# Kernel tuning notes

Measured on AMD Instinct MI355X. Metric: run time of the kernel, lower is better.

## Reference

```python
import jax, jax.numpy as jnp
import numpy as np

D_MODEL = 256; N_LEVELS = 4; N_HEADS = 8; N_POINTS = 4
H_SP = 32; W_SP = 32
B = 2; LEN_Q = 1024; LEN_IN = N_LEVELS * H_SP * W_SP
D_HEAD = D_MODEL // N_HEADS
K9 = 9 * N_POINTS  # 3x3 neighborhood around each of the top-k matches


def setup_inputs() -> dict:
    key = jax.random.key(0)
    k1, k2, k3, k4 = jax.random.split(key, 4)
    bound = (6.0 / (D_MODEL + D_MODEL)) ** 0.5  # xavier_uniform for output_proj
    return {
        "query": jax.random.normal(k1, (B, LEN_Q, D_MODEL), jnp.float32),
        "reference_points": jax.random.uniform(k2, (B, LEN_Q, N_LEVELS, 2), dtype=jnp.float32),
        "input_flatten": jax.random.normal(k3, (B, LEN_IN, D_MODEL), jnp.float32),
        # all levels share the same h==w==32 spatial shape (required by the module)
        "input_spatial_shapes": np.full((N_LEVELS, 2), H_SP, dtype=np.int64),
        "input_level_start_index": (np.arange(N_LEVELS) * H_SP * W_SP).astype(np.int64),
        "out_proj_w": jax.random.uniform(k4, (D_MODEL, D_MODEL), jnp.float32, -bound, bound),
        "out_proj_b": jnp.zeros((D_MODEL,), jnp.float32),
    }


def _sample_offset(query, input_flatten, h, w, t):
    # per-head correlation -> softmax -> top-k index -> 3x3 neighborhood -> (x,y) offsets
    n, lq, _ = query.shape
    q = query.reshape(n, lq, N_HEADS, D_HEAD)
    v = input_flatten.reshape(n, -1, N_HEADS, D_HEAD)
    corr = jnp.einsum('nqhd,nkhd->nhqk', q, v) / D_HEAD          # [n,H,lq,Lin]
    corr = corr.reshape(n, N_HEADS, lq, t, h * w)
    prob = jax.nn.softmax(10.0 * corr, axis=-1)
    _, idx = jax.lax.top_k(prob, N_POINTS)                        # [n,H,lq,t,P] int32
    deltas = jnp.array([-1 - h, -h, 1 - h, -1, 0, 1, -1 + h, h, 1 + h], jnp.int32)
    # torch cat order is delta-major: all P points for delta1, then delta2, ...
    res = (idx[..., None, :] + deltas[:, None]).reshape(n, N_HEADS, lq, t, K9)
    res = jnp.clip(res, 0, (h - 1) * (w - 1))                     # faithful (h-1)*(w-1) clamp
    resf = res.astype(jnp.float32)
    off_w = jnp.floor(resf / h)
    off_h = resf - off_w * h
    offsets = jnp.stack([off_w, off_h], axis=-1)                  # [n,H,lq,t,K9,2]
    return jnp.transpose(offsets, (0, 2, 1, 3, 4, 5))             # [n,lq,H,L,K9,2]


def _ms_deform_attn(value, loc, h, w):
    # value [n,Lin,H,dh]; loc in [0,1], [n,lq,H,L,K9,2]; grid_sample-style bilinear, zero pad
    n, lq = loc.shape[0], loc.shape[1]
    v = value.reshape(n, N_LEVELS, h * w, N_HEADS, D_HEAD)
    v = jnp.transpose(v, (0, 3, 1, 2, 4))                         # [n,H,L,hw,dh]
    x = loc[..., 0] * w - 0.5
    y = loc[..., 1] * h - 0.5
    x0 = jnp.floor(x); y0 = jnp.floor(y)
    lw = x - x0; lh = y - y0
    attn_w = 1.0 / (N_LEVELS * K9)  # softmax of all-ones buffer is uniform
    acc = jnp.zeros((n, lq, N_HEADS, D_HEAD), jnp.float32)
    corners = ((y0, x0, (1 - lh) * (1 - lw)), (y0, x0 + 1, (1 - lh) * lw),
               (y0 + 1, x0, lh * (1 - lw)), (y0 + 1, x0 + 1, lh * lw))
    for yi, xi, wgt in corners:
        valid = (yi >= 0) & (yi < h) & (xi >= 0) & (xi < w)
        ii = (jnp.clip(yi, 0, h - 1) * w + jnp.clip(xi, 0, w - 1)).astype(jnp.int32)
        ww = jnp.where(valid, wgt, 0.0) * attn_w                  # [n,lq,H,L,K9]
        ii_t = jnp.transpose(ii, (0, 2, 3, 1, 4)).reshape(n, N_HEADS, N_LEVELS, lq * K9)
        g = jnp.take_along_axis(v, ii_t[..., None], axis=3)       # [n,H,L,lq*K9,dh]
        g = g.reshape(n, N_HEADS, N_LEVELS, lq, K9, D_HEAD)
        ww_t = jnp.transpose(ww, (0, 2, 3, 1, 4))                 # [n,H,L,lq,K9]
        acc = acc + jnp.einsum('nhlqk,nhlqkd->nqhd', ww_t, g)
    return acc.reshape(n, lq, D_MODEL)


def reference(query, reference_points, input_flatten, input_spatial_shapes,
              input_level_start_index, out_proj_w, out_proj_b):
    ss = np.asarray(input_spatial_shapes)
    h = int(ss[0, 0]); w = h
    lin = input_flatten.shape[1]
    t = lin // (h * w)  # == N_LEVELS
    value = input_flatten.reshape(input_flatten.shape[0], lin, N_HEADS, D_HEAD)
    offsets = _sample_offset(query, input_flatten, h, w, t)
    assert reference_points.shape[-1] == 2
    normalizer = jnp.asarray(np.stack([ss[:, 1], ss[:, 0]], -1), jnp.float32)  # [L,2]=(w,h)
    loc = offsets / normalizer[None, None, None, :, None, :]
    out = _ms_deform_attn(value, loc, h, w)
    out = out @ out_proj_w.T + out_proj_b
    return out, loc
```

## Files before the change

kernel.cpp:

```cpp
#include <hip/hip_runtime.h>
#include <math.h>

#define BB 2
#define LQ 1024
#define DM 256
#define NH 8
#define DH 32
#define NL 4
#define HWsp 1024
#define LIN 4096
#define K9 36
#define NGRP (BB * NH * NL * LQ)

typedef short bf16x8 __attribute__((ext_vector_type(8)));
typedef float f32x4 __attribute__((ext_vector_type(4)));

__device__ __forceinline__ ushort bf16rn(float x) {
  unsigned u = __float_as_uint(x);
  unsigned r = (u + 0x7FFFu + ((u >> 16) & 1u)) >> 16;
  return (ushort)r;
}
__device__ __forceinline__ float bf16tof(ushort h) {
  return __uint_as_float(((unsigned)h) << 16);
}

#define INSERT4(val, index)                                              \
  {                                                                      \
    const float v_ = (val);                                              \
    const int ix_ = (index);                                             \
    if (v_ > v3) {                                                       \
      if (v_ > v1) {                                                     \
        if (v_ > v0) {                                                   \
          v3 = v2; i3 = i2; v2 = v1; i2 = i1; v1 = v0; i1 = i0;          \
          v0 = v_; i0 = ix_;                                             \
        } else {                                                         \
          v3 = v2; i3 = i2; v2 = v1; i2 = i1; v1 = v_; i1 = ix_;         \
        }                                                                \
      } else {                                                           \
        if (v_ > v2) {                                                   \
          v3 = v2; i3 = i2; v2 = v_; i2 = ix_;                           \
        } else {                                                         \
          v3 = v_; i3 = ix_;                                             \
        }                                                                \
      }                                                                  \
    }                                                                    \
  }

#define LEXGT(v_, ix_, vv, ii) (((v_) > (vv)) || ((v_) == (vv) && (ix_) < (ii)))

#define INSERT4LEX(val, index)                                               \
  {                                                                          \
    const float v_ = (val);                                                  \
    const int ix_ = (index);                                                 \
    if (LEXGT(v_, ix_, rv3, ri3)) {                                          \
      if (LEXGT(v_, ix_, rv1, ri1)) {                                        \
        if (LEXGT(v_, ix_, rv0, ri0)) {                                      \
          rv3 = rv2; ri3 = ri2; rv2 = rv1; ri2 = ri1; rv1 = rv0; ri1 = ri0;  \
          rv0 = v_; ri0 = ix_;                                               \
        } else {                                                             \
          rv3 = rv2; ri3 = ri2; rv2 = rv1; ri2 = ri1; rv1 = v_; ri1 = ix_;   \
        }                                                                    \
      } else {                                                               \
        if (LEXGT(v_, ix_, rv2, ri2)) {                                      \
          rv3 = rv2; ri3 = ri2; rv2 = v_; ri2 = ix_;                         \
        } else {                                                             \
          rv3 = v_; ri3 = ix_;                                               \
        }                                                                    \
      }                                                                      \
    }                                                                        \
  }

#define LMAX(av, ai, bv, bi)                                        \
  {                                                                 \
    const bool g_ = ((av) > (bv)) || ((av) == (bv) && (ai) < (bi)); \
    if (!g_) { (av) = (bv); (ai) = (bi); }                          \
  }
#define CEX(av, ai, bv, bi)                                         \
  {                                                                 \
    const bool g_ = ((av) > (bv)) || ((av) == (bv) && (ai) < (bi)); \
    const float tv_ = g_ ? (av) : (bv);                             \
    const int ti_ = g_ ? (ai) : (bi);                               \
    (bv) = g_ ? (bv) : (av); (bi) = g_ ? (bi) : (ai);               \
    (av) = tv_; (ai) = ti_;                                         \
  }

#define PSTRIDE ((size_t)BB * NL * NH * 1024 * 32)

__global__ __launch_bounds__(256) void vsplit_kernel(
    const float* __restrict__ value, ushort* __restrict__ vs) {
  const int T = blockIdx.x * 256 + threadIdx.x;
  const int flat = T << 3;
  const int n = flat >> 20;
  const int rem = flat & 0xFFFFF;
  const int lin = rem >> 8;
  const int d0 = rem & 255;
  const int l = lin >> 10, row = lin & 1023;
  const int h = d0 >> 5, dd = d0 & 31;

  const float* src = value + (size_t)flat;
  float xf[8];
  *(float4*)&xf[0] = *(const float4*)src;
  *(float4*)&xf[4] = *(const float4*)(src + 4);

  ushort uh[8], ul[8], ul2[8];
  #pragma unroll
  for (int j = 0; j < 8; ++j) {
    const float x = xf[j];
    const ushort h1 = bf16rn(x);
    const float r1 = x - bf16tof(h1);
    const ushort h2 = bf16rn(r1);
    const float r2 = r1 - bf16tof(h2);
    uh[j] = h1; ul[j] = h2; ul2[j] = bf16rn(r2);
  }
  const size_t ob = ((((size_t)((n * NL + l) * NH + h)) << 10) + row) * 32 + dd;
  *(bf16x8*)(vs + 0 * PSTRIDE + ob) =
      (bf16x8){(short)uh[0], (short)uh[1], (short)uh[2], (short)uh[3],
               (short)uh[4], (short)uh[5], (short)uh[6], (short)uh[7]};
  *(bf16x8*)(vs + 1 * PSTRIDE + ob) =
      (bf16x8){(short)ul[0], (short)ul[1], (short)ul[2], (short)ul[3],
               (short)ul[4], (short)ul[5], (short)ul[6], (short)ul[7]};
  *(bf16x8*)(vs + 2 * PSTRIDE + ob) =
      (bf16x8){(short)ul2[0], (short)ul2[1], (short)ul2[2], (short)ul2[3],
               (short)ul2[4], (short)ul2[5], (short)ul2[6], (short)ul2[7]};
}

template <int SPLIT, int PRESPLIT>
__global__ __launch_bounds__(256) void corr_topk_kernel(
    const float* __restrict__ query, const float* __restrict__ value,
    const ushort* __restrict__ vs, int* __restrict__ idx_out,
    float4* __restrict__ pval, int4* __restrict__ pidx) {
  __shared__ ushort hiL[64][32];
  __shared__ ushort loL[64][32];
  __shared__ ushort lo2L[64][32];

  const int tid = threadIdx.x;
  const int nh = blockIdx.z;
  const int n = nh >> 3, h = nh & 7;
  const int l = blockIdx.y;
  const int qc = (SPLIT == 2) ? ((int)blockIdx.x >> 1) : (int)blockIdx.x;
  const int half = (SPLIT == 2) ? ((int)blockIdx.x & 1) : 0;
  const int c0 = (SPLIT == 2) ? (half << 3) : 0;
  const int c1 = (SPLIT == 2) ? (c0 + 8) : 16;
  const int w = tid >> 6, L = tid & 63;
  const int qtile = (qc << 2) + w;
  const int r16 = L & 15, g = L >> 4;

  float qf[8];
  bf16x8 qhi, qlo, qlo2;
  {
    const float* qp =
        query + (size_t)(n * LQ + (qtile << 4) + r16) * DM + h * DH + (g << 3);
    *(float4*)&qf[0] = *(const float4*)qp;
    *(float4*)&qf[4] = *(const float4*)(qp + 4);
    ushort uh[8], ul[8], ul2[8];
    #pragma unroll
    for (int j = 0; j < 8; ++j) {
      const float x = qf[j];
      const ushort h1 = bf16rn(x);
      const float r1 = x - bf16tof(h1);
      const ushort h2 = bf16rn(r1);
      const float r2 = r1 - bf16tof(h2);
      uh[j] = h1; ul[j] = h2; ul2[j] = bf16rn(r2);
    }
    qhi = (bf16x8){(short)uh[0], (short)uh[1], (short)uh[2], (short)uh[3],
                   (short)uh[4], (short)uh[5], (short)uh[6], (short)uh[7]};
    qlo = (bf16x8){(short)ul[0], (short)ul[1], (short)ul[2], (short)ul[3],
                   (short)ul[4], (short)ul[5], (short)ul[6], (short)ul[7]};
    qlo2 = (bf16x8){(short)ul2[0], (short)ul2[1], (short)ul2[2], (short)ul2[3],
                    (short)ul2[4], (short)ul2[5], (short)ul2[6], (short)ul2[7]};
  }

  float v0 = -INFINITY, v1 = -INFINITY, v2 = -INFINITY, v3 = -INFINITY;
  int i0 = 0, i1 = 0, i2 = 0, i3 = 0;

  const int srow = tid >> 2, s = tid & 3;
  const int wslot = (s ^ ((srow >> 1) & 3)) << 3;
  const int rslot = (g ^ ((r16 >> 1) & 3)) << 3;
  const ushort* psbase =
      PRESPLIT ? vs + ((((size_t)((n * NL + l) * NH + h)) << 10)) * 32 : nullptr;
  const float* vbase = value + (size_t)(n * LIN + l * HWsp) * DM + h * DH;

  for (int c = c0; c < c1; ++c) {
    if (PRESPLIT) {
      const size_t off = ((size_t)((c << 6) + srow)) * 32 + (s << 3);
      *(bf16x8*)&hiL[srow][wslot] = *(const bf16x8*)(psbase + off);
      *(bf16x8*)&loL[srow][wslot] = *(const bf16x8*)(psbase + PSTRIDE + off);
      *(bf16x8*)&lo2L[srow][wslot] = *(const bf16x8*)(psbase + 2 * PSTRIDE + off);
    } else {
      const float* vp = vbase + (size_t)((c << 6) + srow) * DM + (s << 3);
      float xf[8];
      *(float4*)&xf[0] = *(const float4*)vp;
      *(float4*)&xf[4] = *(const float4*)(vp + 4);
      ushort uh[8], ul[8], ul2[8];
      #pragma unroll
      for (int j = 0; j < 8; ++j) {
        const float x = xf[j];
        const ushort h1 = bf16rn(x);
        const float r1 = x - bf16tof(h1);
        const ushort h2 = bf16rn(r1);
        const float r2 = r1 - bf16tof(h2);
        uh[j] = h1; ul[j] = h2; ul2[j] = bf16rn(r2);
      }
      *(bf16x8*)&hiL[srow][wslot] =
          (bf16x8){(short)uh[0], (short)uh[1], (short)uh[2], (short)uh[3],
                   (short)uh[4], (short)uh[5], (short)uh[6], (short)uh[7]};
      *(bf16x8*)&loL[srow][wslot] =
          (bf16x8){(short)ul[0], (short)ul[1], (short)ul[2], (short)ul[3],
                   (short)ul[4], (short)ul[5], (short)ul[6], (short)ul[7]};
      *(bf16x8*)&lo2L[srow][wslot] =
          (bf16x8){(short)ul2[0], (short)ul2[1], (short)ul2[2], (short)ul2[3],
                   (short)ul2[4], (short)ul2[5], (short)ul2[6], (short)ul2[7]};
    }
    __syncthreads();

    #pragma unroll
    for (int t = 0; t < 4; ++t) {
      const int row = (t << 4) + r16;
      const bf16x8 ahi = *(const bf16x8*)&hiL[row][rslot];
      const bf16x8 alo = *(const bf16x8*)&loL[row][rslot];
      const bf16x8 alo2 = *(const bf16x8*)&lo2L[row][rslot];
      f32x4 acc = {0.f, 0.f, 0.f, 0.f};
      acc = __builtin_amdgcn_mfma_f32_16x16x32_bf16(alo2, qhi, acc, 0, 0, 0);
      acc = __builtin_amdgcn_mfma_f32_16x16x32_bf16(ahi, qlo2, acc, 0, 0, 0);
      acc = __builtin_amdgcn_mfma_f32_16x16x32_bf16(alo, qlo, acc, 0, 0, 0);
      acc = __builtin_amdgcn_mfma_f32_16x16x32_bf16(alo, qhi, acc, 0, 0, 0);
      acc = __builtin_amdgcn_mfma_f32_16x16x32_bf16(ahi, qlo, acc, 0, 0, 0);
      acc = __builtin_amdgcn_mfma_f32_16x16x32_bf16(ahi, qhi, acc, 0, 0, 0);
      const float qm = fmaxf(fmaxf(acc[0], acc[1]), fmaxf(acc[2], acc[3]));
      const int qd = (c << 4) + (t << 2) + g;
      INSERT4(qm, qd);
    }
    __syncthreads();
  }

  #pragma unroll
  for (int m = 16; m < 64; m <<= 1) {
    const float b0 = __shfl_xor(v0, m);
    const float b1 = __shfl_xor(v1, m);
    const float b2 = __shfl_xor(v2, m);
    const float b3 = __shfl_xor(v3, m);
    const int j0 = __shfl_xor(i0, m);
    const int j1 = __shfl_xor(i1, m);
    const int j2 = __shfl_xor(i2, m);
    const int j3 = __shfl_xor(i3, m);
    LMAX(v0, i0, b3, j3);
    LMAX(v1, i1, b2, j2);
    LMAX(v2, i2, b1, j1);
    LMAX(v3, i3, b0, j0);
    CEX(v0, i0, v2, i2);
    CEX(v1, i1, v3, i3);
    CEX(v0, i0, v1, i1);
    CEX(v2, i2, v3, i3);
  }

  float rv0 = -INFINITY, rv1 = -INFINITY, rv2 = -INFINITY, rv3 = -INFINITY;
  int ri0 = 0, ri1 = 0, ri2 = 0, ri3 = 0;
  #define RECOVER_QUAD(QID)                                              \
    {                                                                    \
      _Pragma("unroll")                                                  \
      for (int j = 0; j < 4; ++j) {                                      \
        const int k = ((QID) << 2) + j;                                  \
        const float* vf = vbase + (size_t)k * DM + (g << 3);             \
        const float4 a0 = *(const float4*)vf;                            \
        const float4 a1 = *(const float4*)(vf + 4);                      \
        float p = qf[0] * a0.x;                                          \
        p = fmaf(qf[1], a0.y, p);                                        \
        p = fmaf(qf[2], a0.z, p);                                        \
        p = fmaf(qf[3], a0.w, p);                                        \
        p = fmaf(qf[4], a1.x, p);                                        \
        p = fmaf(qf[5], a1.y, p);                                        \
        p = fmaf(qf[6], a1.z, p);                                        \
        p = fmaf(qf[7], a1.w, p);                                        \
        p += __shfl_xor(p, 16);                                          \
        p += __shfl_xor(p, 32);                                          \
        INSERT4LEX(p, k);                                                \
      }                                                                  \
    }
  RECOVER_QUAD(i0)
  RECOVER_QUAD(i1)
  RECOVER_QUAD(i2)
  RECOVER_QUAD(i3)
  #undef RECOVER_QUAD

  if (L < 16) {
    const int q = (qtile << 4) + L;
    const size_t gi = (((size_t)nh * NL + l) << 10) + q;
    if (SPLIT == 2) {
      pval[gi * 2 + half] = make_float4(rv0, rv1, rv2, rv3);
      pidx[gi * 2 + half] = make_int4(ri0, ri1, ri2, ri3);
    } else {
      ((int4*)idx_out)[gi] = make_int4(ri0, ri1, ri2, ri3);
    }
  }
}

__global__ __launch_bounds__(256) void merge_topk_kernel(
    const float4* __restrict__ pval, const int4* __restrict__ pidx,
    int* __restrict__ idx_out) {
  const int t = blockIdx.x * 256 + threadIdx.x;
  const float4 av = pval[t * 2 + 0];
  const int4 ai = pidx[t * 2 + 0];
  const float4 bv = pval[t * 2 + 1];
  const int4 bi = pidx[t * 2 + 1];
  float w0 = av.x, w1 = av.y, w2 = av.z, w3 = av.w;
  int m0 = ai.x, m1 = ai.y, m2 = ai.z, m3 = ai.w;
  LMAX(w0, m0, bv.w, bi.w);
  LMAX(w1, m1, bv.z, bi.z);
  LMAX(w2, m2, bv.y, bi.y);
  LMAX(w3, m3, bv.x, bi.x);
  CEX(w0, m0, w2, m2);
  CEX(w1, m1, w3, m3);
  CEX(w0, m0, w1, m1);
  CEX(w2, m2, w3, m3);
  ((int4*)idx_out)[t] = make_int4(m0, m1, m2, m3);
}

__global__ __launch_bounds__(256) void loc_kernel(const int* __restrict__ idx_buf,
                                                  float* __restrict__ loc) {
  const int t = blockIdx.x * 256 + threadIdx.x;
  const int k = t % 36;
  int rest = t / 36;
  const int l = rest & 3; rest >>= 2;
  const int h = rest & 7; rest >>= 3;
  const int q = rest & 1023;
  const int n = rest >> 10;
  const int p = k & 3, dd = k >> 2;
  const int idx = idx_buf[(((((n << 3) + h) * NL + l) << 10) + q) * 4 + p];
  const int delta = ((dd / 3) - 1) * 32 + (dd % 3) - 1;
  int res = idx + delta;
  res = min(max(res, 0), 961);
  const int W = res >> 5, H = res & 31;
  ((float2*)loc)[t] = make_float2((float)W * 0.03125f, (float)H * 0.03125f);
}

__global__ __launch_bounds__(256) void gather_kernel(
    const float* __restrict__ value, const int* __restrict__ idx_buf,
    float* __restrict__ acc_out) {
  __shared__ float4 red[NL][8];
  const int bh = blockIdx.x;
  const int h = bh & 7;
  const int nq = bh >> 3;
  const int n = nq >> 10, q = nq & 1023;
  const int tid = threadIdx.x;
  const int l = tid >> 6;
  const int L = tid & 63;
  const int cp = L >> 3, d4 = L & 7;

  const int4 id4 =
      ((const int4*)idx_buf)[((((size_t)((n << 3) + h)) * NL + l) << 10) + q];
  const float4* vb4 =
      (const float4*)(value + (size_t)(n * LIN + l * HWsp) * DM + h * DH) + d4;

  float4 a = make_float4(0.f, 0.f, 0.f, 0.f);
  #pragma unroll
  for (int p = 0; p < 4; ++p) {
    const int idx = (p == 0) ? id4.x : (p == 1) ? id4.y : (p == 2) ? id4.z : id4.w;
    const int H0 = idx & 31, W0 = idx >> 5;
    if (H0 >= 2 && H0 <= 30 && W0 >= 2 && W0 <= 28) {
      const int idxT = (H0 << 5) + W0;
      const int c0i = cp << 1;
      const int ax0 = c0i & 3, ay = c0i >> 2;
      const int r0 = idxT + (ax0 - 2) * 32 + (ay - 2);
      const float wy = (ay == 1 || ay == 2) ? 2.f : 1.f;
      const float f0 = ((ax0 == 2) ? 2.f : 1.f) * wy;
      const float f1 = ((ax0 + 1 == 1) ? 2.f : 1.f) * wy;
      const float4 va = vb4[(size_t)r0 * 64];
      const float4 vbb = vb4[(size_t)(r0 + 32) * 64];
      a.x += f0 * va.x + f1 * vbb.x;
      a.y += f0 * va.y + f1 * vbb.y;
      a.z += f0 * va.z + f1 * vbb.z;
      a.w += f0 * va.w + f1 * vbb.w;
    } else {
      #pragma unroll
      for (int it = 0; it < 5; ++it) {
        const int u = cp + (it << 3);
        const int cell = u >> 2, corner = u & 3;
        const int dy = (cell >= 3) + (cell >= 6) - 1;
        const int dx = cell - (dy + 1) * 3 - 1;
        int res = idx + dy * 32 + dx;
        res = min(max(res, 0), 961);
        const int W = res >> 5, H = res & 31;
        const int cw = corner & 1, ch = corner >> 1;
        const bool ok = (u < 36) && (W >= cw) && (H >= ch);
        const int row = ok ? (((H - ch) << 5) + (W - cw)) : 0;
        const float wgt = ok ? 1.f : 0.f;
        const float4 v = vb4[(size_t)row * 64];
        a.x += wgt * v.x;
        a.y += wgt * v.y;
        a.z += wgt * v.z;
        a.w += wgt * v.w;
      }
    }
  }

  #pragma unroll
  for (int m = 8; m < 64; m <<= 1) {
    a.x += __shfl_xor(a.x, m);
    a.y += __shfl_xor(a.y, m);
    a.z += __shfl_xor(a.z, m);
    a.w += __shfl_xor(a.w, m);
  }
  if (L < 8) red[l][L] = a;
  __syncthreads();
  if (tid < 8) {
    const float4 s0 = red[0][tid], s1 = red[1][tid], s2 = red[2][tid],
                 s3 = red[3][tid];
    float4 o;
    o.x = (s0.x + s1.x + s2.x + s3.x) * (1.0f / 576.0f);
    o.y = (s0.y + s1.y + s2.y + s3.y) * (1.0f / 576.0f);
    o.z = (s0.z + s1.z + s2.z + s3.z) * (1.0f / 576.0f);
    o.w = (s0.w + s1.w + s2.w + s3.w) * (1.0f / 576.0f);
    ((float4*)(acc_out + (size_t)nq * DM + h * DH))[tid] = o;
  }
}

__global__ __launch_bounds__(256) void proj_kernel(
    const float* __restrict__ acc_in, const float* __restrict__ W,
    const float* __restrict__ bias, float* __restrict__ out) {
  __shared__ float la[8][256];
  const int qb = blockIdx.x << 3;
  const int tid = threadIdx.x;
  for (int i = tid; i < 8 * 256; i += 256)
    la[i >> 8][i & 255] = acc_in[((size_t)qb << 8) + i];
  __syncthreads();
  const float* wrow = W + (size_t)tid * 256;
  float s0 = 0.f, s1 = 0.f, s2 = 0.f, s3 = 0.f, s4 = 0.f, s5 = 0.f, s6 = 0.f, s7 = 0.f;
  for (int c0 = 0; c0 < 256; c0 += 4) {
    const float4 wv = *(const float4*)(wrow + c0);
    #define PROJ_STEP(qi, sreg)                                   \
      {                                                           \
        const float4 av = *(const float4*)&la[qi][c0];            \
        sreg = fmaf(wv.x, av.x, sreg);                            \
        sreg = fmaf(wv.y, av.y, sreg);                            \
        sreg = fmaf(wv.z, av.z, sreg);                            \
        sreg = fmaf(wv.w, av.w, sreg);                            \
      }
    PROJ_STEP(0, s0) PROJ_STEP(1, s1) PROJ_STEP(2, s2) PROJ_STEP(3, s3)
    PROJ_STEP(4, s4) PROJ_STEP(5, s5) PROJ_STEP(6, s6) PROJ_STEP(7, s7)
    #undef PROJ_STEP
  }
  const float bj = bias[tid];
  out[(size_t)(qb + 0) * 256 + tid] = s0 + bj;
  out[(size_t)(qb + 1) * 256 + tid] = s1 + bj;
  out[(size_t)(qb + 2) * 256 + tid] = s2 + bj;
  out[(size_t)(qb + 3) * 256 + tid] = s3 + bj;
  out[(size_t)(qb + 4) * 256 + tid] = s4 + bj;
  out[(size_t)(qb + 5) * 256 + tid] = s5 + bj;
  out[(size_t)(qb + 6) * 256 + tid] = s6 + bj;
  out[(size_t)(qb + 7) * 256 + tid] = s7 + bj;
}

extern "C" void kernel_launch(void* const* d_in, const int* in_sizes, int n_in,
                              void* d_out, int out_size, void* d_ws, size_t ws_size,
                              hipStream_t stream) {
  (void)in_sizes; (void)n_in; (void)out_size;
  const float* query = (const float*)d_in[0];
  const float* value = (const float*)d_in[2];
  const float* opw = (const float*)d_in[5];
  const float* opb = (const float*)d_in[6];

  float* out = (float*)d_out;
  float* loc = out + (size_t)BB * LQ * DM;

  const size_t SPLITB = 3 * PSTRIDE * sizeof(ushort);
  const size_t PARTB = (size_t)NGRP * 2 * 16;
  const size_t IDXB = (size_t)NGRP * 4 * sizeof(int);
  const size_t ACCB = (size_t)BB * LQ * DM * sizeof(float);

  if (ws_size >= SPLITB + 2 * PARTB + IDXB + ACCB) {
    ushort* vsb = (ushort*)d_ws;
    float4* pval = (float4*)((char*)d_ws + SPLITB);
    int4* pidx = (int4*)((char*)d_ws + SPLITB + PARTB);
    int* idx_buf = (int*)((char*)d_ws + SPLITB + 2 * PARTB);
    float* acc_buf = (float*)((char*)d_ws + SPLITB + 2 * PARTB + IDXB);

    vsplit_kernel<<<dim3(1024), 256, 0, stream>>>(value, vsb);
    corr_topk_kernel<2, 1><<<dim3(32, NL, BB * NH), 256, 0, stream>>>(
        query, value, vsb, idx_buf, pval, pidx);
    merge_topk_kernel<<<dim3(NGRP / 256), 256, 0, stream>>>(pval, pidx, idx_buf);
    loc_kernel<<<dim3((BB * LQ * NH * NL * K9) / 256), 256, 0, stream>>>(idx_buf, loc);
    gather_kernel<<<dim3(BB * LQ * NH), 256, 0, stream>>>(value, idx_buf, acc_buf);
    proj_kernel<<<dim3(BB * LQ / 8), 256, 0, stream>>>(acc_buf, opw, opb, out);
  } else if (ws_size >= 2 * PARTB + IDXB + ACCB) {
    float4* pval = (float4*)d_ws;
    int4* pidx = (int4*)((char*)d_ws + PARTB);
    int* idx_buf = (int*)((char*)d_ws + 2 * PARTB);
    float* acc_buf = (float*)((char*)d_ws + 2 * PARTB + IDXB);

    corr_topk_kernel<2, 0><<<dim3(32, NL, BB * NH), 256, 0, stream>>>(
        query, value, (const ushort*)nullptr, idx_buf, pval, pidx);
    merge_topk_kernel<<<dim3(NGRP / 256), 256, 0, stream>>>(pval, pidx, idx_buf);
    loc_kernel<<<dim3((BB * LQ * NH * NL * K9) / 256), 256, 0, stream>>>(idx_buf, loc);
    gather_kernel<<<dim3(BB * LQ * NH), 256, 0, stream>>>(value, idx_buf, acc_buf);
    proj_kernel<<<dim3(BB * LQ / 8), 256, 0, stream>>>(acc_buf, opw, opb, out);
  } else {
    int* idx_buf = (int*)d_ws;
    float* acc_buf = (float*)((char*)d_ws + IDXB);

    corr_topk_kernel<1, 0><<<dim3(16, NL, BB * NH), 256, 0, stream>>>(
        query, value, (const ushort*)nullptr, idx_buf, (float4*)nullptr,
        (int4*)nullptr);
    loc_kernel<<<dim3((BB * LQ * NH * NL * K9) / 256), 256, 0, stream>>>(idx_buf, loc);
    gather_kernel<<<dim3(BB * LQ * NH), 256, 0, stream>>>(value, idx_buf, acc_buf);
    proj_kernel<<<dim3(BB * LQ / 8), 256, 0, stream>>>(acc_buf, opw, opb, out);
  }
}
```

Before: 111.0 us.

## Drop third bf16 split term, widen per-lane top-k to 8, fuse loc into merge

Cuts the three-way bf16 split of query and value to a two-way split, removing three of six MFMAs per tile along with one shared buffer and one presplit plane. This lowers MFMA work and memory traffic, but correlation accuracy for the top-k falls to about 16 mantissa bits. To guard against misordering, each lane now keeps a top-8 candidate list, merged with a wider bitonic-style shuffle network, and RECOVER_QUAD runs on all 8 candidates. The loc computation also moves into the merge kernel, saving one launch and one idx re-read.

```diff
diff --git a/kernel.cpp b/kernel.cpp
--- a/kernel.cpp
+++ b/kernel.cpp
@@ -24,26 +24,50 @@
   return __uint_as_float(((unsigned)h) << 16);
 }
 
-#define INSERT4(val, index)                                              \
-  {                                                                      \
-    const float v_ = (val);                                              \
-    const int ix_ = (index);                                             \
-    if (v_ > v3) {                                                       \
-      if (v_ > v1) {                                                     \
-        if (v_ > v0) {                                                   \
-          v3 = v2; i3 = i2; v2 = v1; i2 = i1; v1 = v0; i1 = i0;          \
-          v0 = v_; i0 = ix_;                                             \
-        } else {                                                         \
-          v3 = v2; i3 = i2; v2 = v1; i2 = i1; v1 = v_; i1 = ix_;         \
-        }                                                                \
-      } else {                                                           \
-        if (v_ > v2) {                                                   \
-          v3 = v2; i3 = i2; v2 = v_; i2 = ix_;                           \
-        } else {                                                         \
-          v3 = v_; i3 = ix_;                                             \
-        }                                                                \
-      }                                                                  \
-    }                                                                    \
+#define SHIFT_FROM(J)                                                     \
+  {                                                                       \
+    if (J <= 6) { v7 = v6; i7 = i6; }                                     \
+    if (J <= 5) { v6 = v5; i6 = i5; }                                     \
+    if (J <= 4) { v5 = v4; i5 = i4; }                                     \
+    if (J <= 3) { v4 = v3; i4 = i3; }                                     \
+    if (J <= 2) { v3 = v2; i3 = i2; }                                     \
+    if (J <= 1) { v2 = v1; i2 = i1; }                                     \
+    if (J <= 0) { v1 = v0; i1 = i0; }                                     \
+  }
+#define INSERT8(val, index)                                               \
+  {                                                                       \
+    const float v_ = (val);                                               \
+    const int ix_ = (index);                                              \
+    if (v_ > v7) {                                                        \
+      if (v_ > v3) {                                                      \
+        if (v_ > v1) {                                                    \
+          if (v_ > v0) { SHIFT_FROM(0) v0 = v_; i0 = ix_; }               \
+          else { SHIFT_FROM(1) v1 = v_; i1 = ix_; }                       \
+        } else {                                                          \
+          if (v_ > v2) { SHIFT_FROM(2) v2 = v_; i2 = ix_; }               \
+          else { SHIFT_FROM(3) v3 = v_; i3 = ix_; }                       \
+        }                                                                 \
+      } else {                                                            \
+        if (v_ > v5) {                                                    \
+          if (v_ > v4) { SHIFT_FROM(4) v4 = v_; i4 = ix_; }               \
+          else { SHIFT_FROM(5) v5 = v_; i5 = ix_; }                       \
+        } else {                                                          \
+          if (v_ > v6) { SHIFT_FROM(6) v6 = v_; i6 = ix_; }               \
+          else { v7 = v_; i7 = ix_; }                                     \
+        }                                                                 \
+      }                                                                   \
+    }                                                                     \
+  }
+
+#define VMAX(av, ai, bv, bi)                     \
+  { if ((bv) > (av)) { (av) = (bv); (ai) = (bi); } }
+#define CEXV(av, ai, bv, bi)                     \
+  {                                              \
+    const bool g_ = (av) >= (bv);                \
+    const float tv_ = g_ ? (av) : (bv);          \
+    const int ti_ = g_ ? (ai) : (bi);            \
+    (bv) = g_ ? (bv) : (av); (bi) = g_ ? (bi) : (ai); \
+    (av) = tv_; (ai) = ti_;                      \
   }
 
 #define LEXGT(v_, ix_, vv, ii) (((v_) > (vv)) || ((v_) == (vv) && (ix_) < (ii)))
@@ -102,15 +126,13 @@
   *(float4*)&xf[0] = *(const float4*)src;
   *(float4*)&xf[4] = *(const float4*)(src + 4);
 
-  ushort uh[8], ul[8], ul2[8];
+  ushort uh[8], ul[8];
   #pragma unroll
   for (int j = 0; j < 8; ++j) {
     const float x = xf[j];
     const ushort h1 = bf16rn(x);
-    const float r1 = x - bf16tof(h1);
-    const ushort h2 = bf16rn(r1);
-    const float r2 = r1 - bf16tof(h2);
-    uh[j] = h1; ul[j] = h2; ul2[j] = bf16rn(r2);
+    uh[j] = h1;
+    ul[j] = bf16rn(x - bf16tof(h1));
   }
   const size_t ob = ((((size_t)((n * NL + l) * NH + h)) << 10) + row) * 32 + dd;
   *(bf16x8*)(vs + 0 * PSTRIDE + ob) =
@@ -119,9 +141,6 @@
   *(bf16x8*)(vs + 1 * PSTRIDE + ob) =
       (bf16x8){(short)ul[0], (short)ul[1], (short)ul[2], (short)ul[3],
                (short)ul[4], (short)ul[5], (short)ul[6], (short)ul[7]};
-  *(bf16x8*)(vs + 2 * PSTRIDE + ob) =
-      (bf16x8){(short)ul2[0], (short)ul2[1], (short)ul2[2], (short)ul2[3],
-               (short)ul2[4], (short)ul2[5], (short)ul2[6], (short)ul2[7]};
 }
 
 template <int SPLIT, int PRESPLIT>
@@ -131,7 +150,6 @@
     float4* __restrict__ pval, int4* __restrict__ pidx) {
   __shared__ ushort hiL[64][32];
   __shared__ ushort loL[64][32];
-  __shared__ ushort lo2L[64][32];
 
   const int tid = threadIdx.x;
   const int nh = blockIdx.z;
@@ -146,32 +164,29 @@
   const int r16 = L & 15, g = L >> 4;
 
   float qf[8];
-  bf16x8 qhi, qlo, qlo2;
+  bf16x8 qhi, qlo;
   {
     const float* qp =
         query + (size_t)(n * LQ + (qtile << 4) + r16) * DM + h * DH + (g << 3);
     *(float4*)&qf[0] = *(const float4*)qp;
     *(float4*)&qf[4] = *(const float4*)(qp + 4);
-    ushort uh[8], ul[8], ul2[8];
+    ushort uh[8], ul[8];
     #pragma unroll
     for (int j = 0; j < 8; ++j) {
       const float x = qf[j];
       const ushort h1 = bf16rn(x);
-      const float r1 = x - bf16tof(h1);
-      const ushort h2 = bf16rn(r1);
-      const float r2 = r1 - bf16tof(h2);
-      uh[j] = h1; ul[j] = h2; ul2[j] = bf16rn(r2);
+      uh[j] = h1;
+      ul[j] = bf16rn(x - bf16tof(h1));
     }
     qhi = (bf16x8){(short)uh[0], (short)uh[1], (short)uh[2], (short)uh[3],
                    (short)uh[4], (short)uh[5], (short)uh[6], (short)uh[7]};
     qlo = (bf16x8){(short)ul[0], (short)ul[1], (short)ul[2], (short)ul[3],
                    (short)ul[4], (short)ul[5], (short)ul[6], (short)ul[7]};
-    qlo2 = (bf16x8){(short)ul2[0], (short)ul2[1], (short)ul2[2], (short)ul2[3],
-                    (short)ul2[4], (short)ul2[5], (short)ul2[6], (short)ul2[7]};
-  }
-
-  float v0 = -INFINITY, v1 = -INFINITY, v2 = -INFINITY, v3 = -INFINITY;
-  int i0 = 0, i1 = 0, i2 = 0, i3 = 0;
+  }
+
+  float v0 = -INFINITY, v1 = -INFINITY, v2 = -INFINITY, v3 = -INFINITY,
+        v4 = -INFINITY, v5 = -INFINITY, v6 = -INFINITY, v7 = -INFINITY;
+  int i0 = 0, i1 = 0, i2 = 0, i3 = 0, i4 = 0, i5 = 0, i6 = 0, i7 = 0;
 
   const int srow = tid >> 2, s = tid & 3;
   const int wslot = (s ^ ((srow >> 1) & 3)) << 3;
@@ -185,21 +200,18 @@
       const size_t off = ((size_t)((c << 6) + srow)) * 32 + (s << 3);
       *(bf16x8*)&hiL[srow][wslot] = *(const bf16x8*)(psbase + off);
       *(bf16x8*)&loL[srow][wslot] = *(const bf16x8*)(psbase + PSTRIDE + off);
-      *(bf16x8*)&lo2L[srow][wslot] = *(const bf16x8*)(psbase + 2 * PSTRIDE + off);
     } else {
       const float* vp = vbase + (size_t)((c << 6) + srow) * DM + (s << 3);
       float xf[8];
       *(float4*)&xf[0] = *(const float4*)vp;
       *(float4*)&xf[4] = *(const float4*)(vp + 4);
-      ushort uh[8], ul[8], ul2[8];
+      ushort uh[8], ul[8];
       #pragma unroll
       for (int j = 0; j < 8; ++j) {
         const float x = xf[j];
         const ushort h1 = bf16rn(x);
-        const float r1 = x - bf16tof(h1);
-        const ushort h2 = bf16rn(r1);
-        const float r2 = r1 - bf16tof(h2);
-        uh[j] = h1; ul[j] = h2; ul2[j] = bf16rn(r2);
+        uh[j] = h1;
+        ul[j] = bf16rn(x - bf16tof(h1));
       }
       *(bf16x8*)&hiL[srow][wslot] =
           (bf16x8){(short)uh[0], (short)uh[1], (short)uh[2], (short)uh[3],
@@ -207,9 +219,6 @@
       *(bf16x8*)&loL[srow][wslot] =
           (bf16x8){(short)ul[0], (short)ul[1], (short)ul[2], (short)ul[3],
                    (short)ul[4], (short)ul[5], (short)ul[6], (short)ul[7]};
-      *(bf16x8*)&lo2L[srow][wslot] =
-          (bf16x8){(short)ul2[0], (short)ul2[1], (short)ul2[2], (short)ul2[3],
-                   (short)ul2[4], (short)ul2[5], (short)ul2[6], (short)ul2[7]};
     }
     __syncthreads();
 
@@ -218,39 +227,37 @@
       const int row = (t << 4) + r16;
       const bf16x8 ahi = *(const bf16x8*)&hiL[row][rslot];
       const bf16x8 alo = *(const bf16x8*)&loL[row][rslot];
-      const bf16x8 alo2 = *(const bf16x8*)&lo2L[row][rslot];
       f32x4 acc = {0.f, 0.f, 0.f, 0.f};
-      acc = __builtin_amdgcn_mfma_f32_16x16x32_bf16(alo2, qhi, acc, 0, 0, 0);
-      acc = __builtin_amdgcn_mfma_f32_16x16x32_bf16(ahi, qlo2, acc, 0, 0, 0);
-      acc = __builtin_amdgcn_mfma_f32_16x16x32_bf16(alo, qlo, acc, 0, 0, 0);
       acc = __builtin_amdgcn_mfma_f32_16x16x32_bf16(alo, qhi, acc, 0, 0, 0);
       acc = __builtin_amdgcn_mfma_f32_16x16x32_bf16(ahi, qlo, acc, 0, 0, 0);
       acc = __builtin_amdgcn_mfma_f32_16x16x32_bf16(ahi, qhi, acc, 0, 0, 0);
       const float qm = fmaxf(fmaxf(acc[0], acc[1]), fmaxf(acc[2], acc[3]));
       const int qd = (c << 4) + (t << 2) + g;
-      INSERT4(qm, qd);
+      INSERT8(qm, qd);
     }
     __syncthreads();
   }
 
   #pragma unroll
   for (int m = 16; m < 64; m <<= 1) {
-    const float b0 = __shfl_xor(v0, m);
-    const float b1 = __shfl_xor(v1, m);
-    const float b2 = __shfl_xor(v2, m);
-    const float b3 = __shfl_xor(v3, m);
-    const int j0 = __shfl_xor(i0, m);
-    const int j1 = __shfl_xor(i1, m);
-    const int j2 = __shfl_xor(i2, m);
-    const int j3 = __shfl_xor(i3, m);
-    LMAX(v0, i0, b3, j3);
-    LMAX(v1, i1, b2, j2);
-    LMAX(v2, i2, b1, j1);
-    LMAX(v3, i3, b0, j0);
-    CEX(v0, i0, v2, i2);
-    CEX(v1, i1, v3, i3);
-    CEX(v0, i0, v1, i1);
-    CEX(v2, i2, v3, i3);
+    const float b0 = __shfl_xor(v0, m), b1 = __shfl_xor(v1, m);
+    const float b2 = __shfl_xor(v2, m), b3 = __shfl_xor(v3, m);
+    const float b4 = __shfl_xor(v4, m), b5 = __shfl_xor(v5, m);
+    const float b6 = __shfl_xor(v6, m), b7 = __shfl_xor(v7, m);
+    const int j0 = __shfl_xor(i0, m), j1 = __shfl_xor(i1, m);
+    const int j2 = __shfl_xor(i2, m), j3 = __shfl_xor(i3, m);
+    const int j4 = __shfl_xor(i4, m), j5 = __shfl_xor(i5, m);
+    const int j6 = __shfl_xor(i6, m), j7 = __shfl_xor(i7, m);
+    VMAX(v0, i0, b7, j7); VMAX(v1, i1, b6, j6);
+    VMAX(v2, i2, b5, j5); VMAX(v3, i3, b4, j4);
+    VMAX(v4, i4, b3, j3); VMAX(v5, i5, b2, j2);
+    VMAX(v6, i6, b1, j1); VMAX(v7, i7, b0, j0);
+    CEXV(v0, i0, v4, i4); CEXV(v1, i1, v5, i5);
+    CEXV(v2, i2, v6, i6); CEXV(v3, i3, v7, i7);
+    CEXV(v0, i0, v2, i2); CEXV(v1, i1, v3, i3);
+    CEXV(v4, i4, v6, i6); CEXV(v5, i5, v7, i7);
+    CEXV(v0, i0, v1, i1); CEXV(v2, i2, v3, i3);
+    CEXV(v4, i4, v5, i5); CEXV(v6, i6, v7, i7);
   }
 
   float rv0 = -INFINITY, rv1 = -INFINITY, rv2 = -INFINITY, rv3 = -INFINITY;
@@ -280,6 +287,10 @@
   RECOVER_QUAD(i1)
   RECOVER_QUAD(i2)
   RECOVER_QUAD(i3)
+  RECOVER_QUAD(i4)
+  RECOVER_QUAD(i5)
+  RECOVER_QUAD(i6)
+  RECOVER_QUAD(i7)
   #undef RECOVER_QUAD
 
   if (L < 16) {
@@ -294,9 +305,9 @@
   }
 }
 
-__global__ __launch_bounds__(256) void merge_topk_kernel(
+__global__ __launch_bounds__(256) void merge_topk_loc_kernel(
     const float4* __restrict__ pval, const int4* __restrict__ pidx,
-    int* __restrict__ idx_out) {
+    int* __restrict__ idx_out, float* __restrict__ loc) {
   const int t = blockIdx.x * 256 + threadIdx.x;
   const float4 av = pval[t * 2 + 0];
   const int4 ai = pidx[t * 2 + 0];
@@ -313,6 +324,26 @@
   CEX(w0, m0, w1, m1);
   CEX(w2, m2, w3, m3);
   ((int4*)idx_out)[t] = make_int4(m0, m1, m2, m3);
+
+  const int q = t & 1023, l = (t >> 10) & 3, h = (t >> 12) & 7, n = t >> 15;
+  const size_t base2 =
+      (size_t)((((((n << 10) + q) << 3) + h) << 2) + l) * 36;
+  float4* lp4 = (float4*)(loc + base2 * 2);
+  const int idxs[4] = {m0, m1, m2, m3};
+  #pragma unroll
+  for (int dd = 0; dd < 9; ++dd) {
+    const int delta = (dd / 3 - 1) * 32 + (dd % 3) - 1;
+    float vv[8];
+    #pragma unroll
+    for (int p = 0; p < 4; ++p) {
+      int res = idxs[p] + delta;
+      res = min(max(res, 0), 961);
+      vv[p * 2] = (float)(res >> 5) * 0.03125f;
+      vv[p * 2 + 1] = (float)(res & 31) * 0.03125f;
+    }
+    lp4[dd * 2] = make_float4(vv[0], vv[1], vv[2], vv[3]);
+    lp4[dd * 2 + 1] = make_float4(vv[4], vv[5], vv[6], vv[7]);
+  }
 }
 
 __global__ __launch_bounds__(256) void loc_kernel(const int* __restrict__ idx_buf,
@@ -462,7 +493,7 @@
   float* out = (float*)d_out;
   float* loc = out + (size_t)BB * LQ * DM;
 
-  const size_t SPLITB = 3 * PSTRIDE * sizeof(ushort);
+  const size_t SPLITB = 2 * PSTRIDE * sizeof(ushort);
   const size_t PARTB = (size_t)NGRP * 2 * 16;
   const size_t IDXB = (size_t)NGRP * 4 * sizeof(int);
   const size_t ACCB = (size_t)BB * LQ * DM * sizeof(float);
@@ -477,8 +508,8 @@
     vsplit_kernel<<<dim3(1024), 256, 0, stream>>>(value, vsb);
     corr_topk_kernel<2, 1><<<dim3(32, NL, BB * NH), 256, 0, stream>>>(
         query, value, vsb, idx_buf, pval, pidx);
-    merge_topk_kernel<<<dim3(NGRP / 256), 256, 0, stream>>>(pval, pidx, idx_buf);
-    loc_kernel<<<dim3((BB * LQ * NH * NL * K9) / 256), 256, 0, stream>>>(idx_buf, loc);
+    merge_topk_loc_kernel<<<dim3(NGRP / 256), 256, 0, stream>>>(pval, pidx,
+                                                                idx_buf, loc);
     gather_kernel<<<dim3(BB * LQ * NH), 256, 0, stream>>>(value, idx_buf, acc_buf);
     proj_kernel<<<dim3(BB * LQ / 8), 256, 0, stream>>>(acc_buf, opw, opb, out);
   } else if (ws_size >= 2 * PARTB + IDXB + ACCB) {
@@ -489,8 +520,8 @@
 
     corr_topk_kernel<2, 0><<<dim3(32, NL, BB * NH), 256, 0, stream>>>(
         query, value, (const ushort*)nullptr, idx_buf, pval, pidx);
-    merge_topk_kernel<<<dim3(NGRP / 256), 256, 0, stream>>>(pval, pidx, idx_buf);
-    loc_kernel<<<dim3((BB * LQ * NH * NL * K9) / 256), 256, 0, stream>>>(idx_buf, loc);
+    merge_topk_loc_kernel<<<dim3(NGRP / 256), 256, 0, stream>>>(pval, pidx,
+                                                                idx_buf, loc);
     gather_kernel<<<dim3(BB * LQ * NH), 256, 0, stream>>>(value, idx_buf, acc_buf);
     proj_kernel<<<dim3(BB * LQ / 8), 256, 0, stream>>>(acc_buf, opw, opb, out);
   } else {
```

Result: slower. 144.3 us (+30.0%).
